# Kernel tuning notes

Hardware: AMD Instinct MI355X
Metric: run time of the kernel (lower is better)

The kernel has to match this reference:

```python
import jax, jax.numpy as jnp
import numpy as np

NHEAD = 16


def corrcoef(X, Y):
    # X, Y: [..., S, D]; Pearson correlation between rows of X and rows of Y
    X = X - X.mean(-1, keepdims=True)
    Y = Y - Y.mean(-1, keepdims=True)
    c = jnp.einsum('...id,...jd->...ij', X, Y)            # [..., S, S]
    d = jnp.einsum('...id,...id->...i', X, Y)             # diagonal of c
    stddev = jnp.sqrt(d)
    c = c / stddev[..., :, None]
    c = c / stddev[..., None, :]
    c = jnp.clip(c, -1.0, 1.0)
    return jnp.where(jnp.isnan(c), 0.0, c)


def setup_inputs() -> dict:
    key = jax.random.key(0)
    k1, k2, k3 = jax.random.split(key, 3)
    T, B, D = 2048, 2, 1024
    query = jax.random.normal(k1, (T, B, D), dtype=jnp.float32)
    W_qkv = jax.random.normal(k2, (3 * D, D), dtype=jnp.float32) * (1.0 / np.sqrt(D))
    b_qkv = jax.random.normal(k3, (3 * D,), dtype=jnp.float32) * 0.01
    return {"query": query, "W_qkv": W_qkv, "b_qkv": b_qkv}


def reference(query, W_qkv, b_qkv):
    T, B, D = query.shape
    hd = D // NHEAD
    qkv = query @ W_qkv.T + b_qkv                          # [T, B, 3D]
    q, k, v = jnp.split(qkv, 3, axis=-1)

    def to_bhsd(x):
        return x.reshape(T, B, NHEAD, hd).transpose(1, 2, 0, 3)  # [B, H, S, hd]

    q, k, v = to_bhsd(q), to_bhsd(k), to_bhsd(v)
    corr = corrcoef(q, k)                                   # [B, H, S, S]
    corr = jax.nn.softmax(corr, axis=-1)                    # eval: dropout_p = 0
    return corr @ v                                         # [B, H, S, hd]
```

## Files before the change

### kernel.cpp

```cpp
#include <hip/hip_runtime.h>

#define S 2048
#define D 1024
#define NH 16
#define HD 64
#define N3 3072
#define M 4096

typedef short s16x8 __attribute__((ext_vector_type(8)));
typedef _Float16 f16x8 __attribute__((ext_vector_type(8)));
typedef _Float16 f16x2 __attribute__((ext_vector_type(2)));
typedef float f32x4 __attribute__((ext_vector_type(4)));
typedef unsigned int u32;
typedef u32 u32x4 __attribute__((ext_vector_type(4)));

__device__ __forceinline__ unsigned short f2bf(float f) {
  unsigned u = __builtin_bit_cast(unsigned, f);
  u += 0x7fffu + ((u >> 16) & 1u);
  return (unsigned short)(u >> 16);
}
__device__ __forceinline__ float bf2f(unsigned short h) {
  return __builtin_bit_cast(float, (unsigned)h << 16);
}
__device__ __forceinline__ unsigned short f2h(float f) {
  _Float16 h = (_Float16)f;
  return __builtin_bit_cast(unsigned short, h);
}

__device__ __forceinline__ float wsum(float v) {
  #pragma unroll
  for (int m = 1; m < 64; m <<= 1) v += __shfl_xor(v, m, 64);
  return v;
}

__device__ __forceinline__ void gload_lds16(const unsigned short* g, unsigned short* l) {
  __builtin_amdgcn_global_load_lds(
      (const __attribute__((address_space(1))) u32*)g,
      (__attribute__((address_space(3))) u32*)l, 16, 0, 0);
}

__global__ __launch_bounds__(256) void split_k(const float* __restrict__ q,
                                               const float* __restrict__ w,
                                               unsigned short* __restrict__ A1,
                                               unsigned short* __restrict__ A2,
                                               unsigned short* __restrict__ W1,
                                               unsigned short* __restrict__ W2) {
  const size_t gid = (size_t)blockIdx.x * 256 + threadIdx.x;
  const size_t NA = (size_t)M * D / 4;
  float4 x;
  unsigned short* p1; unsigned short* p2; size_t qi; float scale;
  if (gid < NA) {
    qi = gid;  x = ((const float4*)q)[qi];
    p1 = A1; p2 = A2; scale = 64.f;
  } else {
    qi = gid - NA;  x = ((const float4*)w)[qi];
    p1 = W1; p2 = W2; scale = 1024.f;
  }
  float e[4] = {x.x * scale, x.y * scale, x.z * scale, x.w * scale};
  unsigned short h1[4], h2[4];
  #pragma unroll
  for (int i = 0; i < 4; ++i) {
    _Float16 a = (_Float16)e[i];
    float r = e[i] - (float)a;
    _Float16 b = (_Float16)r;
    h1[i] = __builtin_bit_cast(unsigned short, a);
    h2[i] = __builtin_bit_cast(unsigned short, b);
  }
  *(ushort4*)&p1[qi * 4] = make_ushort4(h1[0], h1[1], h1[2], h1[3]);
  *(ushort4*)&p2[qi * 4] = make_ushort4(h2[0], h2[1], h2[2], h2[3]);
}

__global__ __launch_bounds__(256) void gemm_mfma(const unsigned short* __restrict__ A1,
                                                 const unsigned short* __restrict__ A2,
                                                 const unsigned short* __restrict__ W1,
                                                 const unsigned short* __restrict__ W2,
                                                 const float* __restrict__ bias,
                                                 float* __restrict__ C) {
  __shared__ unsigned short As[128 * 64];
  __shared__ unsigned short Bs[128 * 64];
  const int tid = threadIdx.x;
  const int w = tid >> 6, l = tid & 63;
  const int lo = l & 15, hi = l >> 4;
  const int n0 = blockIdx.x * 128, m0 = blockIdx.y * 128;
  const int wr = w >> 1, wc = w & 1;

  const int nseg = (n0 >= 2048) ? 1 : 3;

  const int srow = (tid >> 3) & 31;
  const int skc = tid & 7;

  f32x4 acc[4][4];
  #pragma unroll
  for (int mi = 0; mi < 4; ++mi)
    #pragma unroll
    for (int nj = 0; nj < 4; ++nj) acc[mi][nj] = (f32x4){0.f, 0.f, 0.f, 0.f};

  for (int s = 0; s < 3; ++s) {
    if (s >= nseg) break;
    const unsigned short* Ab;
    const unsigned short* Bb;
    switch (s) {
      case 0: Ab = A1; Bb = W1; break;
      case 1: Ab = A2; Bb = W1; break;
      default: Ab = A1; Bb = W2; break;
    }
    Ab += (size_t)m0 * D;
    Bb += (size_t)n0 * D;

    for (int k0 = 0; k0 < D; k0 += 64) {
      __syncthreads();
      #pragma unroll
      for (int c = 0; c < 4; ++c) {
        const int row = c * 32 + srow;
        const int koct = skc ^ (row & 7);
        gload_lds16(Ab + (size_t)row * D + k0 + koct * 8,
                    As + c * 2048 + w * 512);
        gload_lds16(Bb + (size_t)row * D + k0 + koct * 8,
                    Bs + c * 2048 + w * 512);
      }
      __syncthreads();

      f16x8 af[4][2], bf[4][2];
      #pragma unroll
      for (int mi = 0; mi < 4; ++mi)
        #pragma unroll
        for (int ks = 0; ks < 2; ++ks) {
          const int row = wr * 64 + mi * 16 + lo;
          const int koct = (ks * 4 + hi) ^ (lo & 7);
          af[mi][ks] = *(const f16x8*)&As[row * 64 + koct * 8];
        }
      #pragma unroll
      for (int nj = 0; nj < 4; ++nj)
        #pragma unroll
        for (int ks = 0; ks < 2; ++ks) {
          const int row = wc * 64 + nj * 16 + lo;
          const int koct = (ks * 4 + hi) ^ (lo & 7);
          bf[nj][ks] = *(const f16x8*)&Bs[row * 64 + koct * 8];
        }
      #pragma unroll
      for (int mi = 0; mi < 4; ++mi)
        #pragma unroll
        for (int nj = 0; nj < 4; ++nj)
          #pragma unroll
          for (int ks = 0; ks < 2; ++ks)
            acc[mi][nj] = __builtin_amdgcn_mfma_f32_16x16x32_f16(
                af[mi][ks], bf[nj][ks], acc[mi][nj], 0, 0, 0);
    }
  }

  #pragma unroll
  for (int mi = 0; mi < 4; ++mi)
    #pragma unroll
    for (int nj = 0; nj < 4; ++nj) {
      const int n = n0 + wc * 64 + nj * 16 + lo;
      const float bj = bias[n];
      #pragma unroll
      for (int r = 0; r < 4; ++r) {
        const int m = m0 + wr * 64 + mi * 16 + hi * 4 + r;
        C[(size_t)m * N3 + n] = acc[mi][nj][r] * (1.f / 65536.f) + bj;
      }
    }
}

__global__ __launch_bounds__(256) void stats_k(const float* __restrict__ qkv,
                                               unsigned short* __restrict__ qhi,
                                               unsigned short* __restrict__ qlo,
                                               unsigned short* __restrict__ khi,
                                               unsigned short* __restrict__ klo,
                                               unsigned short* __restrict__ vt) {
  __shared__ unsigned short VsT[64][65];
  const int tt = blockIdx.x, bh = blockIdx.y;
  const int b = bh >> 4, h = bh & 15;
  const int w = threadIdx.x >> 6, l = threadIdx.x & 63;

  for (int rr = 0; rr < 16; ++rr) {
    const int t = tt * 64 + w * 16 + rr;
    const size_t base = (size_t)(t * 2 + b) * N3 + h * HD;
    const float q = qkv[base + l];
    const float k = qkv[base + D + l];
    const float v = qkv[base + 2 * D + l];
    const float qm = wsum(q) * (1.f / 64.f);
    const float km = wsum(k) * (1.f / 64.f);
    const float qcv = q - qm, kcv = k - km;
    const float d = wsum(qcv * kcv);
    float rv = 0.f;
    if (d > 0.f) {
      rv = rsqrtf(d);
      rv = rv * (1.5f - 0.5f * d * rv * rv);
    }
    const float qn = qcv * rv, kn = kcv * rv;
    const size_t ro = ((size_t)bh * S + t) * HD + l;
    const unsigned short qh = f2bf(qn);
    const unsigned short kh = f2bf(kn);
    qhi[ro] = qh;  qlo[ro] = f2bf(qn - bf2f(qh));
    khi[ro] = kh;  klo[ro] = f2bf(kn - bf2f(kh));
    VsT[l][w * 16 + rr] = f2h(v);
  }
  __syncthreads();
  const int dd = threadIdx.x >> 2, seg = threadIdx.x & 3;
  unsigned pk[8];
  #pragma unroll
  for (int e = 0; e < 8; ++e) {
    unsigned l2 = VsT[dd][seg * 16 + 2 * e];
    unsigned h2 = VsT[dd][seg * 16 + 2 * e + 1];
    pk[e] = l2 | (h2 << 16);
  }
  unsigned short* dst = vt + ((size_t)bh * HD + dd) * S + tt * 64 + seg * 16;
  *(uint4*)dst       = make_uint4(pk[0], pk[1], pk[2], pk[3]);
  *(uint4*)(dst + 8) = make_uint4(pk[4], pk[5], pk[6], pk[7]);
}

__global__ __launch_bounds__(512, 4) void attn_k(const unsigned short* __restrict__ qhi,
                                                 const unsigned short* __restrict__ qlo,
                                                 const unsigned short* __restrict__ khi,
                                                 const unsigned short* __restrict__ klo,
                                                 const unsigned short* __restrict__ vt,
                                                 float* __restrict__ out) {
  __shared__ unsigned short Kh[64 * 64];
  __shared__ unsigned short Kl[64 * 64];
  __shared__ unsigned short Vsm[64 * 64];

  const int tid = threadIdx.x;
  const int w = tid >> 6, l = tid & 63;
  const int lo = l & 15, hi = l >> 4;

  const int wgid = blockIdx.x;
  const int orig = (wgid & 7) * 64 + (wgid >> 3);
  const int bh = orig >> 4, qt = orig & 15;

  const unsigned short* qhb = qhi + (size_t)bh * S * HD;
  const unsigned short* qlb = qlo + (size_t)bh * S * HD;
  const unsigned short* khb = khi + (size_t)bh * S * HD;
  const unsigned short* klb = klo + (size_t)bh * S * HD;
  const unsigned short* vbase = vt + (size_t)bh * HD * S;
  const int qrow0 = qt * 128 + w * 16;

  const int srow = tid >> 3;
  const int sg = (tid & 7) ^ (srow & 7);

  s16x8 aqh[2], aql[2];
  #pragma unroll
  for (int ks = 0; ks < 2; ++ks) {
    const size_t off = (size_t)(qrow0 + lo) * HD + ks * 32 + hi * 8;
    aqh[ks] = *(const s16x8*)(qhb + off);
    aql[ks] = *(const s16x8*)(qlb + off);
  }

  f32x4 oacc[4];
  float den = 0.f;
  #pragma unroll
  for (int nd = 0; nd < 4; ++nd) oacc[nd] = (f32x4){0.f, 0.f, 0.f, 0.f};

  const int sel = hi >> 1;
  const int srcA = lo + ((hi & 1) << 5);
  const int srcB = srcA + 16;

  for (int j0 = 0; j0 < S; j0 += 64) {
    __syncthreads();
    {
      const size_t kgo = (size_t)(j0 + srow) * HD + sg * 8;
      gload_lds16(khb + kgo, Kh + w * 512);
      gload_lds16(klb + kgo, Kl + w * 512);
      gload_lds16(vbase + (size_t)srow * S + j0 + sg * 8, Vsm + w * 512);
    }
    __syncthreads();

    u32 pk2[4][2];
    #pragma unroll
    for (int nj = 0; nj < 4; ++nj) {
      f32x4 acc = (f32x4){0.f, 0.f, 0.f, 0.f};
      #pragma unroll
      for (int ks = 0; ks < 2; ++ks) {
        const int off = (nj * 16 + lo) * 64 + (((ks * 4 + hi) ^ (lo & 7)) << 3);
        s16x8 akh = *(const s16x8*)&Kh[off];
        s16x8 akl = *(const s16x8*)&Kl[off];
        acc = __builtin_amdgcn_mfma_f32_16x16x32_bf16(akh, aqh[ks], acc, 0, 0, 0);
        acc = __builtin_amdgcn_mfma_f32_16x16x32_bf16(akl, aqh[ks], acc, 0, 0, 0);
        acc = __builtin_amdgcn_mfma_f32_16x16x32_bf16(akh, aql[ks], acc, 0, 0, 0);
      }
      float e[4];
      #pragma unroll
      for (int r = 0; r < 4; ++r) {
        float c = fminf(1.f, fmaxf(-1.f, acc[r]));
        e[r] = __expf(c);
        den += e[r];
      }
      pk2[nj][0] = __builtin_bit_cast(u32, __builtin_amdgcn_cvt_pkrtz(e[0], e[1]));
      pk2[nj][1] = __builtin_bit_cast(u32, __builtin_amdgcn_cvt_pkrtz(e[2], e[3]));
    }

    f16x8 pa[2];
    #pragma unroll
    for (int ks = 0; ks < 2; ++ks) {
      u32 a0 = __shfl(pk2[2 * ks][0], srcA, 64);
      u32 b0 = __shfl(pk2[2 * ks + 1][0], srcA, 64);
      u32 a1 = __shfl(pk2[2 * ks][1], srcA, 64);
      u32 b1 = __shfl(pk2[2 * ks + 1][1], srcA, 64);
      u32 a2 = __shfl(pk2[2 * ks][0], srcB, 64);
      u32 b2 = __shfl(pk2[2 * ks + 1][0], srcB, 64);
      u32 a3 = __shfl(pk2[2 * ks][1], srcB, 64);
      u32 b3 = __shfl(pk2[2 * ks + 1][1], srcB, 64);
      u32x4 u;
      u[0] = sel ? b0 : a0;
      u[1] = sel ? b1 : a1;
      u[2] = sel ? b2 : a2;
      u[3] = sel ? b3 : a3;
      pa[ks] = __builtin_bit_cast(f16x8, u);
    }

    #pragma unroll
    for (int nd = 0; nd < 4; ++nd) {
      const int vrow = nd * 16 + lo;
      f16x8 bv0 = *(const f16x8*)&Vsm[vrow * 64 + ((hi ^ (lo & 7)) << 3)];
      f16x8 bv1 = *(const f16x8*)&Vsm[vrow * 64 + (((4 + hi) ^ (lo & 7)) << 3)];
      oacc[nd] = __builtin_amdgcn_mfma_f32_16x16x32_f16(pa[0], bv0, oacc[nd], 0, 0, 0);
      oacc[nd] = __builtin_amdgcn_mfma_f32_16x16x32_f16(pa[1], bv1, oacc[nd], 0, 0, 0);
    }
  }

  float d1 = den + __shfl_xor(den, 16, 64);
  float dtot = d1 + __shfl_xor(d1, 32, 64);
  float inv = 1.f / dtot;
  float dr[4];
  #pragma unroll
  for (int r = 0; r < 4; ++r) dr[r] = __shfl(inv, hi * 4 + r, 64);

  #pragma unroll
  for (int nd = 0; nd < 4; ++nd)
    #pragma unroll
    for (int r = 0; r < 4; ++r) {
      const size_t row = (size_t)bh * S + qrow0 + hi * 4 + r;
      out[row * HD + nd * 16 + lo] = oacc[nd][r] * dr[r];
    }
}

extern "C" void kernel_launch(void* const* d_in, const int* in_sizes, int n_in,
                              void* d_out, int out_size, void* d_ws, size_t ws_size,
                              hipStream_t stream) {
  const float* query = (const float*)d_in[0];
  const float* W     = (const float*)d_in[1];
  const float* bias  = (const float*)d_in[2];
  float* out = (float*)d_out;
  char* ws = (char*)d_ws;

  float*          qkv = (float*)ws;
  unsigned short* A1 = (unsigned short*)(ws + 50331648);
  unsigned short* A2 = (unsigned short*)(ws + 58720256);
  unsigned short* W1 = (unsigned short*)(ws + 67108864);
  unsigned short* W2 = (unsigned short*)(ws + 73400320);
  unsigned short* qhi = (unsigned short*)(ws + 50331648);
  unsigned short* qlo = (unsigned short*)(ws + 58720256);
  unsigned short* khi = (unsigned short*)(ws + 67108864);
  unsigned short* klo = (unsigned short*)(ws + 75497472);
  unsigned short* vt  = (unsigned short*)(ws + 83886080);

  split_k  <<<dim3(7168), 256, 0, stream>>>(query, W, A1, A2, W1, W2);
  gemm_mfma<<<dim3(24, 32), 256, 0, stream>>>(A1, A2, W1, W2, bias, qkv);
  stats_k  <<<dim3(32, 32), 256, 0, stream>>>(qkv, qhi, qlo, khi, klo, vt);
  attn_k   <<<dim3(512), 512, 0, stream>>>(qhi, qlo, khi, klo, vt, out);
}
```

Before: 176.6 us.

## Split attention over key halves with a combine pass and deferred correlation scaling

The attention kernel now splits each query tile's key range into two halves, doubling the grid to 1024 workgroups. Each half writes an unnormalized partial output and a partial softmax denominator, and a new combine kernel sums the halves and normalizes. The per-row inverse-stddev factor is no longer baked into the stored bf16 hi/lo Q and K; it is saved per row, staged into LDS per key tile, and applied to the dot product before clamping. The change also adds s_setprio around the compute section and drops the occupancy hint from launch bounds. The aim is more parallelism and better CU occupancy, at the cost of an extra launch and roughly 48MB of extra partial-output memory traffic.

```diff
diff --git a/kernel.cpp b/kernel.cpp
--- a/kernel.cpp
+++ b/kernel.cpp
@@ -9,7 +9,6 @@
 
 typedef short s16x8 __attribute__((ext_vector_type(8)));
 typedef _Float16 f16x8 __attribute__((ext_vector_type(8)));
-typedef _Float16 f16x2 __attribute__((ext_vector_type(2)));
 typedef float f32x4 __attribute__((ext_vector_type(4)));
 typedef unsigned int u32;
 typedef u32 u32x4 __attribute__((ext_vector_type(4)));
@@ -37,6 +36,11 @@
   __builtin_amdgcn_global_load_lds(
       (const __attribute__((address_space(1))) u32*)g,
       (__attribute__((address_space(3))) u32*)l, 16, 0, 0);
+}
+__device__ __forceinline__ void gload_lds4(const float* g, float* l) {
+  __builtin_amdgcn_global_load_lds(
+      (const __attribute__((address_space(1))) u32*)g,
+      (__attribute__((address_space(3))) u32*)l, 4, 0, 0);
 }
 
 __global__ __launch_bounds__(256) void split_k(const float* __restrict__ q,
@@ -167,7 +171,8 @@
                                                unsigned short* __restrict__ qlo,
                                                unsigned short* __restrict__ khi,
                                                unsigned short* __restrict__ klo,
-                                               unsigned short* __restrict__ vt) {
+                                               unsigned short* __restrict__ vt,
+                                               float* __restrict__ rs) {
   __shared__ unsigned short VsT[64][65];
   const int tt = blockIdx.x, bh = blockIdx.y;
   const int b = bh >> 4, h = bh & 15;
@@ -188,12 +193,12 @@
       rv = rsqrtf(d);
       rv = rv * (1.5f - 0.5f * d * rv * rv);
     }
-    const float qn = qcv * rv, kn = kcv * rv;
     const size_t ro = ((size_t)bh * S + t) * HD + l;
-    const unsigned short qh = f2bf(qn);
-    const unsigned short kh = f2bf(kn);
-    qhi[ro] = qh;  qlo[ro] = f2bf(qn - bf2f(qh));
-    khi[ro] = kh;  klo[ro] = f2bf(kn - bf2f(kh));
+    const unsigned short qh = f2bf(qcv);
+    const unsigned short kh = f2bf(kcv);
+    qhi[ro] = qh;  qlo[ro] = f2bf(qcv - bf2f(qh));
+    khi[ro] = kh;  klo[ro] = f2bf(kcv - bf2f(kh));
+    if (l == 0) rs[(size_t)bh * S + t] = rv;
     VsT[l][w * 16 + rr] = f2h(v);
   }
   __syncthreads();
@@ -210,29 +215,35 @@
   *(uint4*)(dst + 8) = make_uint4(pk[4], pk[5], pk[6], pk[7]);
 }
 
-__global__ __launch_bounds__(512, 4) void attn_k(const unsigned short* __restrict__ qhi,
-                                                 const unsigned short* __restrict__ qlo,
-                                                 const unsigned short* __restrict__ khi,
-                                                 const unsigned short* __restrict__ klo,
-                                                 const unsigned short* __restrict__ vt,
-                                                 float* __restrict__ out) {
+__global__ __launch_bounds__(512) void attn_k(const unsigned short* __restrict__ qhi,
+                                              const unsigned short* __restrict__ qlo,
+                                              const unsigned short* __restrict__ khi,
+                                              const unsigned short* __restrict__ klo,
+                                              const unsigned short* __restrict__ vt,
+                                              const float* __restrict__ rs,
+                                              float* __restrict__ O0,
+                                              float* __restrict__ O1,
+                                              float* __restrict__ D0,
+                                              float* __restrict__ D1) {
   __shared__ unsigned short Kh[64 * 64];
   __shared__ unsigned short Kl[64 * 64];
   __shared__ unsigned short Vsm[64 * 64];
+  __shared__ float Rsl[64];
 
   const int tid = threadIdx.x;
   const int w = tid >> 6, l = tid & 63;
   const int lo = l & 15, hi = l >> 4;
 
   const int wgid = blockIdx.x;
-  const int orig = (wgid & 7) * 64 + (wgid >> 3);
-  const int bh = orig >> 4, qt = orig & 15;
+  const int orig = (wgid & 7) * 128 + (wgid >> 3);
+  const int bh = orig >> 5, qt = (orig >> 1) & 15, half = orig & 1;
 
   const unsigned short* qhb = qhi + (size_t)bh * S * HD;
   const unsigned short* qlb = qlo + (size_t)bh * S * HD;
   const unsigned short* khb = khi + (size_t)bh * S * HD;
   const unsigned short* klb = klo + (size_t)bh * S * HD;
   const unsigned short* vbase = vt + (size_t)bh * HD * S;
+  const float* rbase = rs + (size_t)bh * S;
   const int qrow0 = qt * 128 + w * 16;
 
   const int srow = tid >> 3;
@@ -245,6 +256,7 @@
     aqh[ks] = *(const s16x8*)(qhb + off);
     aql[ks] = *(const s16x8*)(qlb + off);
   }
+  const float rsq = rbase[qrow0 + lo];
 
   f32x4 oacc[4];
   float den = 0.f;
@@ -255,16 +267,19 @@
   const int srcA = lo + ((hi & 1) << 5);
   const int srcB = srcA + 16;
 
-  for (int j0 = 0; j0 < S; j0 += 64) {
+  const int jbeg = half * 1024;
+  for (int j0 = jbeg; j0 < jbeg + 1024; j0 += 64) {
     __syncthreads();
     {
       const size_t kgo = (size_t)(j0 + srow) * HD + sg * 8;
       gload_lds16(khb + kgo, Kh + w * 512);
       gload_lds16(klb + kgo, Kl + w * 512);
       gload_lds16(vbase + (size_t)srow * S + j0 + sg * 8, Vsm + w * 512);
+      if (w == 0) gload_lds4(rbase + j0 + l, Rsl);
     }
     __syncthreads();
 
+    __builtin_amdgcn_s_setprio(1);
     u32 pk2[4][2];
     #pragma unroll
     for (int nj = 0; nj < 4; ++nj) {
@@ -281,7 +296,8 @@
       float e[4];
       #pragma unroll
       for (int r = 0; r < 4; ++r) {
-        float c = fminf(1.f, fmaxf(-1.f, acc[r]));
+        const float rj = Rsl[nj * 16 + hi * 4 + r];
+        float c = fminf(1.f, fmaxf(-1.f, acc[r] * rsq * rj));
         e[r] = __expf(c);
         den += e[r];
       }
@@ -316,22 +332,39 @@
       oacc[nd] = __builtin_amdgcn_mfma_f32_16x16x32_f16(pa[0], bv0, oacc[nd], 0, 0, 0);
       oacc[nd] = __builtin_amdgcn_mfma_f32_16x16x32_f16(pa[1], bv1, oacc[nd], 0, 0, 0);
     }
-  }
+    __builtin_amdgcn_s_setprio(0);
+  }
+
+  float* Oh = half ? O1 : O0;
+  float* Dh = half ? D1 : D0;
 
   float d1 = den + __shfl_xor(den, 16, 64);
   float dtot = d1 + __shfl_xor(d1, 32, 64);
-  float inv = 1.f / dtot;
-  float dr[4];
-  #pragma unroll
-  for (int r = 0; r < 4; ++r) dr[r] = __shfl(inv, hi * 4 + r, 64);
+  if (hi == 0) Dh[(size_t)bh * S + qrow0 + lo] = dtot;
 
   #pragma unroll
   for (int nd = 0; nd < 4; ++nd)
     #pragma unroll
     for (int r = 0; r < 4; ++r) {
       const size_t row = (size_t)bh * S + qrow0 + hi * 4 + r;
-      out[row * HD + nd * 16 + lo] = oacc[nd][r] * dr[r];
-    }
+      Oh[row * HD + nd * 16 + lo] = oacc[nd][r];
+    }
+}
+
+__global__ __launch_bounds__(256) void combine_k(const float* __restrict__ O0,
+                                                 const float* __restrict__ O1,
+                                                 const float* __restrict__ D0,
+                                                 const float* __restrict__ D1,
+                                                 float* __restrict__ out) {
+  const size_t i4 = (size_t)blockIdx.x * 256 + threadIdx.x;
+  const size_t row = i4 >> 4;
+  float4 a = ((const float4*)O0)[i4];
+  float4 b = ((const float4*)O1)[i4];
+  const float inv = 1.f / (D0[row] + D1[row]);
+  float4 o;
+  o.x = (a.x + b.x) * inv;  o.y = (a.y + b.y) * inv;
+  o.z = (a.z + b.z) * inv;  o.w = (a.w + b.w) * inv;
+  ((float4*)out)[i4] = o;
 }
 
 extern "C" void kernel_launch(void* const* d_in, const int* in_sizes, int n_in,
@@ -344,6 +377,10 @@
   char* ws = (char*)d_ws;
 
   float*          qkv = (float*)ws;
+  float* O0 = (float*)ws;
+  float* O1 = (float*)(ws + 16777216);
+  float* Dp0 = (float*)(ws + 33554432);
+  float* Dp1 = (float*)(ws + 33816576);
   unsigned short* A1 = (unsigned short*)(ws + 50331648);
   unsigned short* A2 = (unsigned short*)(ws + 58720256);
   unsigned short* W1 = (unsigned short*)(ws + 67108864);
@@ -353,9 +390,11 @@
   unsigned short* khi = (unsigned short*)(ws + 67108864);
   unsigned short* klo = (unsigned short*)(ws + 75497472);
   unsigned short* vt  = (unsigned short*)(ws + 83886080);
+  float*          rsb = (float*)(ws + 92274688);
 
   split_k  <<<dim3(7168), 256, 0, stream>>>(query, W, A1, A2, W1, W2);
   gemm_mfma<<<dim3(24, 32), 256, 0, stream>>>(A1, A2, W1, W2, bias, qkv);
-  stats_k  <<<dim3(32, 32), 256, 0, stream>>>(qkv, qhi, qlo, khi, klo, vt);
-  attn_k   <<<dim3(512), 512, 0, stream>>>(qhi, qlo, khi, klo, vt, out);
-}
+  stats_k  <<<dim3(32, 32), 256, 0, stream>>>(qkv, qhi, qlo, khi, klo, vt, rsb);
+  attn_k   <<<dim3(1024), 512, 0, stream>>>(qhi, qlo, khi, klo, vt, rsb, O0, O1, Dp0, Dp1);
+  combine_k<<<dim3(4096), 256, 0, stream>>>(O0, O1, Dp0, Dp1, out);
+}
```

New measurement: 188.8 us. 1.07x slower.
